# Kernel tuning notes

Hardware: AMD Instinct MI355X
Metric: run time of the kernel (lower is better)

## Reference

```python
import jax, jax.numpy as jnp
import numpy as np

C = 16  # CHANNELS
SOBEL_X = jnp.array([[-1., 0., 1.], [-2., 0., 2.], [-1., 0., 1.]], dtype=jnp.float32)
SOBEL_Y = SOBEL_X.T


def _depthwise3x3(x, k3):
    # x: [B,C,H,W]; k3: [3,3] kernel applied per-channel (groups=C, padding=1)
    k = jnp.broadcast_to(k3[None, None], (C, 1, 3, 3))
    return jax.lax.conv_general_dilated(x, k, window_strides=(1, 1), padding='SAME',
                                        feature_group_count=C)


def _alive_mask(x):
    # max_pool2d(alpha, k=3, s=1, p=1) > 0.1 on channel 3
    alpha = x[:, 3:4]
    pooled = jax.lax.reduce_window(alpha, -jnp.inf, jax.lax.max,
                                   (1, 1, 3, 3), (1, 1, 1, 1), 'SAME')
    return pooled > 0.1


def setup_inputs() -> dict:
    key = jax.random.key(0)
    k0, k1, k2, k3 = jax.random.split(key, 4)
    B = 1024
    state_grid = jax.random.uniform(k0, (B, C, 32, 32), dtype=jnp.float32)
    rand_mask = jax.random.randint(k1, (B, 1, 32, 32), 0, 2, dtype=jnp.int32)
    # dense_128: Conv2d(48, 128, k=1); torch default kaiming-uniform-ish -> use scaled normal
    w1 = jax.random.normal(k2, (128, 48), dtype=jnp.float32) * (1.0 / np.sqrt(48.0))
    b1 = jnp.zeros((128,), dtype=jnp.float32)
    # dense_16: original zero-init; use small random weights for a non-degenerate baseline
    w2 = jax.random.normal(k3, (16, 128), dtype=jnp.float32) * 0.01
    b2 = jnp.zeros((16,), dtype=jnp.float32)
    return {"state_grid": state_grid, "rand_mask": rand_mask,
            "w1": w1, "b1": b1, "w2": w2, "b2": b2}


def reference(state_grid, rand_mask, w1, b1, w2, b2):
    # perceive: depthwise sobel-x, sobel-y, identity -> concat to 48 channels
    px = _depthwise3x3(state_grid, SOBEL_X)
    py = _depthwise3x3(state_grid, SOBEL_Y)
    perception = jnp.concatenate([px, py, state_grid], axis=1)  # [B,48,32,32]
    # 1x1 conv MLP
    h = jax.nn.relu(jnp.einsum('oc,bchw->bohw', w1, perception) + b1[None, :, None, None])
    dx = jnp.einsum('oc,bchw->bohw', w2, h) + b2[None, :, None, None]  # [B,16,32,32]
    # stochastic update (0/1 mask broadcast over channels)
    x = state_grid + dx * rand_mask.astype(state_grid.dtype)
    # alive masking
    alive = _alive_mask(state_grid) & _alive_mask(x)
    x = x * alive.astype(state_grid.dtype)
    return jnp.clip(x, 0.0, 1.0)
```

## Files before the change

### kernel.cpp

```cpp
#include <hip/hip_runtime.h>
#include <hip/hip_bf16.h>

#define TPB 256

typedef __attribute__((ext_vector_type(8))) short short8v;
typedef __attribute__((ext_vector_type(4))) float f32x4;

__device__ __forceinline__ unsigned short f2bf(float f) {
    union { __hip_bfloat16 b; unsigned short u; } cv;
    cv.b = __float2bfloat16(f);
    return cv.u;
}
__device__ __forceinline__ float bf2f(unsigned int u) {
    return __uint_as_float(u << 16);
}
__device__ __forceinline__ unsigned int packbf(float x, float y) {
    return (unsigned int)f2bf(x) | ((unsigned int)f2bf(y) << 16);
}

__global__ __launch_bounds__(TPB, 2) void nca_mfma(
    const float* __restrict__ state,
    const int*   __restrict__ rmask,
    const float* __restrict__ w1,
    const float* __restrict__ b1,
    const float* __restrict__ w2,
    const float* __restrict__ b2,
    float* __restrict__ out)
{
    __shared__ __align__(16) unsigned short sSt[16 * 34 * 36];
    __shared__ __align__(16) unsigned short sP [64 * 72];
    __shared__ __align__(16) unsigned short sH [64 * 136];
    __shared__ __align__(16) float          sA [34 * 34];
    __shared__ unsigned char                sPre[1024];

    const int b    = blockIdx.x;
    const int tid  = threadIdx.x;
    const int lane = tid & 63;
    const int wv   = tid >> 6;
    const int lr   = lane & 15;
    const int lg   = lane >> 4;

    short8v w1f[8][2];
    short8v w2f[4];
    float   b1v[8];
    #pragma unroll
    for (int n = 0; n < 8; ++n) {
        const int f = lr * 8 + n;
        #pragma unroll
        for (int kk = 0; kk < 2; ++kk) {
            const int k0 = kk * 32 + lg * 8;
            short8v v;
            if (k0 < 48) {
                const float4 x0 = *reinterpret_cast<const float4*>(w1 + f * 48 + k0);
                const float4 x1 = *reinterpret_cast<const float4*>(w1 + f * 48 + k0 + 4);
                v[0]=(short)f2bf(x0.x); v[1]=(short)f2bf(x0.y); v[2]=(short)f2bf(x0.z); v[3]=(short)f2bf(x0.w);
                v[4]=(short)f2bf(x1.x); v[5]=(short)f2bf(x1.y); v[6]=(short)f2bf(x1.z); v[7]=(short)f2bf(x1.w);
            } else {
                #pragma unroll
                for (int e = 0; e < 8; ++e) v[e] = 0;
            }
            w1f[n][kk] = v;
        }
        b1v[n] = b1[f];
    }
    #pragma unroll
    for (int ks = 0; ks < 4; ++ks) {
        const int k0 = ks * 32 + lg * 8;
        const float4 x0 = *reinterpret_cast<const float4*>(w2 + lr * 128 + k0);
        const float4 x1 = *reinterpret_cast<const float4*>(w2 + lr * 128 + k0 + 4);
        short8v v;
        v[0]=(short)f2bf(x0.x); v[1]=(short)f2bf(x0.y); v[2]=(short)f2bf(x0.z); v[3]=(short)f2bf(x0.w);
        v[4]=(short)f2bf(x1.x); v[5]=(short)f2bf(x1.y); v[6]=(short)f2bf(x1.z); v[7]=(short)f2bf(x1.w);
        w2f[ks] = v;
    }
    const float b2v = b2[lr];

    for (int i = tid; i < 16*34*36/2; i += TPB) reinterpret_cast<unsigned int*>(sSt)[i] = 0u;
    for (int i = tid; i < 64*72/2;    i += TPB) reinterpret_cast<unsigned int*>(sP)[i]  = 0u;
    for (int i = tid; i < 34*34;      i += TPB) sA[i] = 0.f;
    __syncthreads();

    const float* gs = state + (size_t)b * 16384;
    #pragma unroll
    for (int k = 0; k < 16; ++k) {
        const int q = tid + k * TPB;
        const float4 v = reinterpret_cast<const float4*>(gs)[q];
        const int c = q >> 8, rem = q & 255;
        const int h = rem >> 3, wg = rem & 7;
        const int eo = c * 1224 + (h + 1) * 36 + (wg * 4 + 2);
        reinterpret_cast<unsigned int*>(&sSt[eo])[0] = packbf(v.x, v.y);
        reinterpret_cast<unsigned int*>(&sSt[eo])[1] = packbf(v.z, v.w);
    }
    __syncthreads();

    for (int p = tid; p < 1024; p += TPB) {
        const int h = p >> 5, w = p & 31;
        const unsigned short* sa = &sSt[3 * 1224 + h * 36 + (w + 1)];
        float m =          bf2f(sa[0]);
        m = fmaxf(m, bf2f(sa[1]));  m = fmaxf(m, bf2f(sa[2]));
        m = fmaxf(m, bf2f(sa[36])); m = fmaxf(m, bf2f(sa[37])); m = fmaxf(m, bf2f(sa[38]));
        m = fmaxf(m, bf2f(sa[72])); m = fmaxf(m, bf2f(sa[73])); m = fmaxf(m, bf2f(sa[74]));
        sPre[p] = (m > 0.1f) ? 1 : 0;
    }

    auto do_gate = [&](int pb, const float* xp) {
        float av = 0.f;
        if (lane < 16) {
            const int p = pb + lane;
            const int h = p >> 5, w = p & 31;
            const float* sa = &sA[h * 34 + w];
            float m =          sa[0];
            m = fmaxf(m, sa[1]);  m = fmaxf(m, sa[2]);
            m = fmaxf(m, sa[34]); m = fmaxf(m, sa[35]); m = fmaxf(m, sa[36]);
            m = fmaxf(m, sa[68]); m = fmaxf(m, sa[69]); m = fmaxf(m, sa[70]);
            av = ((m > 0.1f) && (sPre[p] != 0)) ? 1.f : 0.f;
        }
        const float g0 = __shfl(av, lg * 4 + 0);
        const float g1 = __shfl(av, lg * 4 + 1);
        const float g2 = __shfl(av, lg * 4 + 2);
        const float g3 = __shfl(av, lg * 4 + 3);
        float4 ov;
        ov.x = g0 * fminf(fmaxf(xp[0], 0.f), 1.f);
        ov.y = g1 * fminf(fmaxf(xp[1], 0.f), 1.f);
        ov.z = g2 * fminf(fmaxf(xp[2], 0.f), 1.f);
        ov.w = g3 * fminf(fmaxf(xp[3], 0.f), 1.f);
        *reinterpret_cast<float4*>(&out[(size_t)b * 16384 + lr * 1024 + pb + lg * 4]) = ov;
    };

    float xp[4];
    int pbase_prev = 0;

    for (int s = 0; s < 16; ++s) {
        {
            const int cg = tid & 7;
            const int pp = tid >> 3;
            const int c0 = cg * 2;
            const int hloc = pp >> 4;
            const int h  = s * 2 + hloc;
            const int w0 = (pp & 15) * 2;
            const int j0 = hloc * 32 + w0;
            float sx0[2], sx1[2], sy0[2], sy1[2], id0[2], id1[2];
            #pragma unroll
            for (int ci = 0; ci < 2; ++ci) {
                const unsigned short* bp = &sSt[(c0 + ci) * 1224 + h * 36 + w0];
                float A[3], Bv[3], Cv[3], D[3];
                #pragma unroll
                for (int dr = 0; dr < 3; ++dr) {
                    const unsigned int* rp = reinterpret_cast<const unsigned int*>(bp + dr * 36);
                    const unsigned int u0 = rp[0], u1 = rp[1], u2 = rp[2];
                    A[dr]  = bf2f(u0 >> 16);
                    Bv[dr] = bf2f(u1 & 0xffffu);
                    Cv[dr] = bf2f(u1 >> 16);
                    D[dr]  = bf2f(u2 & 0xffffu);
                }
                const float csa = A[0]  + 2.f * A[1]  + A[2];
                const float csb = Bv[0] + 2.f * Bv[1] + Bv[2];
                const float csc = Cv[0] + 2.f * Cv[1] + Cv[2];
                const float csd = D[0]  + 2.f * D[1]  + D[2];
                sx0[ci] = csc - csa;
                sx1[ci] = csd - csb;
                sy0[ci] = (A[2] + 2.f * Bv[2] + Cv[2]) - (A[0] + 2.f * Bv[0] + Cv[0]);
                sy1[ci] = (Bv[2] + 2.f * Cv[2] + D[2]) - (Bv[0] + 2.f * Cv[0] + D[0]);
                id0[ci] = Bv[1];
                id1[ci] = Cv[1];
            }
            unsigned int* r0 = reinterpret_cast<unsigned int*>(&sP[j0 * 72 + c0]);
            unsigned int* r1 = reinterpret_cast<unsigned int*>(&sP[(j0 + 1) * 72 + c0]);
            r0[0]  = packbf(sx0[0], sx0[1]);
            r0[8]  = packbf(sy0[0], sy0[1]);
            r0[16] = packbf(id0[0], id0[1]);
            r1[0]  = packbf(sx1[0], sx1[1]);
            r1[8]  = packbf(sy1[0], sy1[1]);
            r1[16] = packbf(id1[0], id1[1]);
        }
        __syncthreads();

        f32x4 acc1[8];
        #pragma unroll
        for (int n = 0; n < 8; ++n) { acc1[n][0]=0.f; acc1[n][1]=0.f; acc1[n][2]=0.f; acc1[n][3]=0.f; }
        #pragma unroll
        for (int kk = 0; kk < 2; ++kk) {
            const short8v a = *reinterpret_cast<const short8v*>(&sP[(wv * 16 + lr) * 72 + kk * 32 + lg * 8]);
            #pragma unroll
            for (int n = 0; n < 8; ++n)
                acc1[n] = __builtin_amdgcn_mfma_f32_16x16x32_bf16(a, w1f[n][kk], acc1[n], 0, 0, 0);
        }
        #pragma unroll
        for (int r = 0; r < 4; ++r) {
            const int row = wv * 16 + lg * 4 + r;
            unsigned int pk0, pk1, pk2, pk3;
            pk0 = packbf(fmaxf(acc1[0][r] + b1v[0], 0.f), fmaxf(acc1[1][r] + b1v[1], 0.f));
            pk1 = packbf(fmaxf(acc1[2][r] + b1v[2], 0.f), fmaxf(acc1[3][r] + b1v[3], 0.f));
            pk2 = packbf(fmaxf(acc1[4][r] + b1v[4], 0.f), fmaxf(acc1[5][r] + b1v[5], 0.f));
            pk3 = packbf(fmaxf(acc1[6][r] + b1v[6], 0.f), fmaxf(acc1[7][r] + b1v[7], 0.f));
            uint4 u; u.x = pk0; u.y = pk1; u.z = pk2; u.w = pk3;
            *reinterpret_cast<uint4*>(&sH[row * 136 + lr * 8]) = u;
        }
        __syncthreads();

        f32x4 acc2; acc2[0]=0.f; acc2[1]=0.f; acc2[2]=0.f; acc2[3]=0.f;
        #pragma unroll
        for (int ksx = 0; ksx < 4; ++ksx) {
            const short8v a2 = *reinterpret_cast<const short8v*>(&sH[(wv * 16 + lr) * 136 + ksx * 32 + lg * 8]);
            acc2 = __builtin_amdgcn_mfma_f32_16x16x32_bf16(a2, w2f[ksx], acc2, 0, 0, 0);
        }
        const int pbase = s * 64 + wv * 16;
        const int4   mi  = *reinterpret_cast<const int4*>(&rmask[b * 1024 + pbase + lg * 4]);
        const float4 idv = *reinterpret_cast<const float4*>(&state[(size_t)b * 16384 + lr * 1024 + pbase + lg * 4]);
        float xv[4];
        xv[0] = fmaf(acc2[0] + b2v, (float)mi.x, idv.x);
        xv[1] = fmaf(acc2[1] + b2v, (float)mi.y, idv.y);
        xv[2] = fmaf(acc2[2] + b2v, (float)mi.z, idv.z);
        xv[3] = fmaf(acc2[3] + b2v, (float)mi.w, idv.w);
        if (lr == 3) {
            const int p0 = pbase + lg * 4;
            const int h2 = p0 >> 5, w2c = p0 & 31;
            float* dst = &sA[(h2 + 1) * 34 + (w2c + 1)];
            dst[0] = xv[0]; dst[1] = xv[1]; dst[2] = xv[2]; dst[3] = xv[3];
        }
        __syncthreads();

        if (s > 0) do_gate(pbase_prev, xp);
        xp[0] = xv[0]; xp[1] = xv[1]; xp[2] = xv[2]; xp[3] = xv[3];
        pbase_prev = pbase;
    }
    do_gate(pbase_prev, xp);
}

extern "C" void kernel_launch(void* const* d_in, const int* in_sizes, int n_in,
                              void* d_out, int out_size, void* d_ws, size_t ws_size,
                              hipStream_t stream) {
    const float* state = (const float*)d_in[0];
    const int*   rmask = (const int*)d_in[1];
    const float* w1    = (const float*)d_in[2];
    const float* b1    = (const float*)d_in[3];
    const float* w2    = (const float*)d_in[4];
    const float* b2    = (const float*)d_in[5];
    float* outp = (float*)d_out;

    const int B = in_sizes[0] / (16 * 32 * 32);
    hipLaunchKernelGGL(nca_mfma, dim3(B), dim3(TPB), 0, stream,
                       state, rmask, w1, b1, w2, b2, outp);
}
```

Measured before the change: 187.8 us.

## Make perception and MLP stages wave-local to drop barriers; use hardware bf16 packing

Perception threads are remapped so each wave writes exactly the 16 pixel rows of the shared perception and hidden buffers that its own MFMAs later read. This makes two of the three per-step block barriers unnecessary. The alive-mask gating is pushed back two steps with a double-buffered register copy, so the single remaining barrier still orders the cross-wave alpha reads. Software float-to-bf16 conversion is replaced by the v_cvt_pk_bf16_f32 instruction via inline asm. The rmask and state loads are hoisted to the top of each step so their latency can overlap the compute. In exchange, more registers are kept live and correctness now depends on intra-wave LDS ordering.

```diff
diff --git a/kernel.cpp b/kernel.cpp
--- a/kernel.cpp
+++ b/kernel.cpp
@@ -6,16 +6,19 @@
 typedef __attribute__((ext_vector_type(8))) short short8v;
 typedef __attribute__((ext_vector_type(4))) float f32x4;
 
-__device__ __forceinline__ unsigned short f2bf(float f) {
-    union { __hip_bfloat16 b; unsigned short u; } cv;
-    cv.b = __float2bfloat16(f);
-    return cv.u;
-}
 __device__ __forceinline__ float bf2f(unsigned int u) {
     return __uint_as_float(u << 16);
 }
 __device__ __forceinline__ unsigned int packbf(float x, float y) {
-    return (unsigned int)f2bf(x) | ((unsigned int)f2bf(y) << 16);
+    unsigned int r;
+    asm("v_cvt_pk_bf16_f32 %0, %1, %2" : "=v"(r) : "v"(x), "v"(y));
+    return r;
+}
+__device__ __forceinline__ short8v pack8(float4 a, float4 bq) {
+    union { unsigned int u[4]; short8v s; } c;
+    c.u[0] = packbf(a.x, a.y);  c.u[1] = packbf(a.z, a.w);
+    c.u[2] = packbf(bq.x, bq.y); c.u[3] = packbf(bq.z, bq.w);
+    return c.s;
 }
 
 __global__ __launch_bounds__(TPB, 2) void nca_mfma(
@@ -49,17 +52,14 @@
         #pragma unroll
         for (int kk = 0; kk < 2; ++kk) {
             const int k0 = kk * 32 + lg * 8;
-            short8v v;
             if (k0 < 48) {
                 const float4 x0 = *reinterpret_cast<const float4*>(w1 + f * 48 + k0);
                 const float4 x1 = *reinterpret_cast<const float4*>(w1 + f * 48 + k0 + 4);
-                v[0]=(short)f2bf(x0.x); v[1]=(short)f2bf(x0.y); v[2]=(short)f2bf(x0.z); v[3]=(short)f2bf(x0.w);
-                v[4]=(short)f2bf(x1.x); v[5]=(short)f2bf(x1.y); v[6]=(short)f2bf(x1.z); v[7]=(short)f2bf(x1.w);
+                w1f[n][kk] = pack8(x0, x1);
             } else {
-                #pragma unroll
-                for (int e = 0; e < 8; ++e) v[e] = 0;
+                short8v z = {0,0,0,0,0,0,0,0};
+                w1f[n][kk] = z;
             }
-            w1f[n][kk] = v;
         }
         b1v[n] = b1[f];
     }
@@ -68,10 +68,7 @@
         const int k0 = ks * 32 + lg * 8;
         const float4 x0 = *reinterpret_cast<const float4*>(w2 + lr * 128 + k0);
         const float4 x1 = *reinterpret_cast<const float4*>(w2 + lr * 128 + k0 + 4);
-        short8v v;
-        v[0]=(short)f2bf(x0.x); v[1]=(short)f2bf(x0.y); v[2]=(short)f2bf(x0.z); v[3]=(short)f2bf(x0.w);
-        v[4]=(short)f2bf(x1.x); v[5]=(short)f2bf(x1.y); v[6]=(short)f2bf(x1.z); v[7]=(short)f2bf(x1.w);
-        w2f[ks] = v;
+        w2f[ks] = pack8(x0, x1);
     }
     const float b2v = b2[lr];
 
@@ -127,18 +124,21 @@
         *reinterpret_cast<float4*>(&out[(size_t)b * 16384 + lr * 1024 + pb + lg * 4]) = ov;
     };
 
-    float xp[4];
-    int pbase_prev = 0;
+    float xq[2][4];
 
     for (int s = 0; s < 16; ++s) {
+        const int pbase = s * 64 + wv * 16;
+        const int4   mi  = *reinterpret_cast<const int4*>(&rmask[b * 1024 + pbase + lg * 4]);
+        const float4 idv = *reinterpret_cast<const float4*>(&state[(size_t)b * 16384 + lr * 1024 + pbase + lg * 4]);
+
         {
-            const int cg = tid & 7;
-            const int pp = tid >> 3;
-            const int c0 = cg * 2;
-            const int hloc = pp >> 4;
-            const int h  = s * 2 + hloc;
-            const int w0 = (pp & 15) * 2;
-            const int j0 = hloc * 32 + w0;
+            const int cg   = lane & 7;
+            const int pl   = lane >> 3;
+            const int c0   = cg * 2;
+            const int hloc = wv >> 1;
+            const int w0   = (wv & 1) * 16 + pl * 2;
+            const int h    = s * 2 + hloc;
+            const int j0   = hloc * 32 + w0;
             float sx0[2], sx1[2], sy0[2], sy1[2], id0[2], id1[2];
             #pragma unroll
             for (int ci = 0; ci < 2; ++ci) {
@@ -173,7 +173,6 @@
             r1[8]  = packbf(sy1[0], sy1[1]);
             r1[16] = packbf(id1[0], id1[1]);
         }
-        __syncthreads();
 
         f32x4 acc1[8];
         #pragma unroll
@@ -188,15 +187,13 @@
         #pragma unroll
         for (int r = 0; r < 4; ++r) {
             const int row = wv * 16 + lg * 4 + r;
-            unsigned int pk0, pk1, pk2, pk3;
-            pk0 = packbf(fmaxf(acc1[0][r] + b1v[0], 0.f), fmaxf(acc1[1][r] + b1v[1], 0.f));
-            pk1 = packbf(fmaxf(acc1[2][r] + b1v[2], 0.f), fmaxf(acc1[3][r] + b1v[3], 0.f));
-            pk2 = packbf(fmaxf(acc1[4][r] + b1v[4], 0.f), fmaxf(acc1[5][r] + b1v[5], 0.f));
-            pk3 = packbf(fmaxf(acc1[6][r] + b1v[6], 0.f), fmaxf(acc1[7][r] + b1v[7], 0.f));
-            uint4 u; u.x = pk0; u.y = pk1; u.z = pk2; u.w = pk3;
+            uint4 u;
+            u.x = packbf(fmaxf(acc1[0][r] + b1v[0], 0.f), fmaxf(acc1[1][r] + b1v[1], 0.f));
+            u.y = packbf(fmaxf(acc1[2][r] + b1v[2], 0.f), fmaxf(acc1[3][r] + b1v[3], 0.f));
+            u.z = packbf(fmaxf(acc1[4][r] + b1v[4], 0.f), fmaxf(acc1[5][r] + b1v[5], 0.f));
+            u.w = packbf(fmaxf(acc1[6][r] + b1v[6], 0.f), fmaxf(acc1[7][r] + b1v[7], 0.f));
             *reinterpret_cast<uint4*>(&sH[row * 136 + lr * 8]) = u;
         }
-        __syncthreads();
 
         f32x4 acc2; acc2[0]=0.f; acc2[1]=0.f; acc2[2]=0.f; acc2[3]=0.f;
         #pragma unroll
@@ -204,9 +201,6 @@
             const short8v a2 = *reinterpret_cast<const short8v*>(&sH[(wv * 16 + lr) * 136 + ksx * 32 + lg * 8]);
             acc2 = __builtin_amdgcn_mfma_f32_16x16x32_bf16(a2, w2f[ksx], acc2, 0, 0, 0);
         }
-        const int pbase = s * 64 + wv * 16;
-        const int4   mi  = *reinterpret_cast<const int4*>(&rmask[b * 1024 + pbase + lg * 4]);
-        const float4 idv = *reinterpret_cast<const float4*>(&state[(size_t)b * 16384 + lr * 1024 + pbase + lg * 4]);
         float xv[4];
         xv[0] = fmaf(acc2[0] + b2v, (float)mi.x, idv.x);
         xv[1] = fmaf(acc2[1] + b2v, (float)mi.y, idv.y);
@@ -218,13 +212,15 @@
             float* dst = &sA[(h2 + 1) * 34 + (w2c + 1)];
             dst[0] = xv[0]; dst[1] = xv[1]; dst[2] = xv[2]; dst[3] = xv[3];
         }
+
+        const int par = s & 1;
+        if (s >= 2) do_gate((s - 2) * 64 + wv * 16, xq[par]);
+        xq[par][0] = xv[0]; xq[par][1] = xv[1]; xq[par][2] = xv[2]; xq[par][3] = xv[3];
+
         __syncthreads();
-
-        if (s > 0) do_gate(pbase_prev, xp);
-        xp[0] = xv[0]; xp[1] = xv[1]; xp[2] = xv[2]; xp[3] = xv[3];
-        pbase_prev = pbase;
-    }
-    do_gate(pbase_prev, xp);
+    }
+    do_gate(14 * 64 + wv * 16, xq[0]);
+    do_gate(15 * 64 + wv * 16, xq[1]);
 }
 
 extern "C" void kernel_launch(void* const* d_in, const int* in_sizes, int n_in,
```

After: 190.2 us. No clear change (+1.3%).
